# Optimization experiments

Measured on AMD Instinct MI355X. Metric: run time of the kernel, lower is better.

Reference implementation:

```python
import jax, jax.numpy as jnp
import numpy as np

D = 16  # attention temperature
COEF = 1.0 / float(np.sqrt(D))


def squash2(x, axis=-1):
    sq = jnp.sum(x * x, axis=axis, keepdims=True)
    norm = jnp.sqrt(sq)
    # (1 - 1/exp(||x||)) * x / sqrt(||x||^2 + 1e-8)
    return (1.0 - jnp.exp(-norm)) * x / jnp.sqrt(sq + 1e-8)


def setup_inputs() -> dict:
    key = jax.random.key(0)
    k1, k2, k3 = jax.random.split(key, 3)
    batch, in_caps, in_dim, num_caps, dim_caps = 128, 1024, 16, 16, 16
    x = jax.random.normal(k1, (batch, in_caps, in_dim), dtype=jnp.float32)
    W = 0.01 * jax.random.normal(k2, (1, num_caps, in_caps, dim_caps, in_dim), dtype=jnp.float32)
    B = 0.01 * jax.random.normal(k3, (num_caps, 1, in_caps), dtype=jnp.float32)
    return {"x": x, "W": W, "B": B}


def reference(x, W, B):
    # u_hat[b,n,c,d] = W[n,c,d,:] . x[b,c,:]
    u_hat = jnp.einsum('ncdi,bci->bncd', W[0], x)
    # a = coef * u_hat @ u_hat^T is only consumed via a.sum(dim=-2);
    # sum_r <u_hat[r], u_hat[k]> == <sum_r u_hat[r], u_hat[k]> (same math, no [c,c] matrix)
    scores = COEF * jnp.einsum('bnd,bnkd->bnk', u_hat.sum(axis=2), u_hat)  # [b,n,c]
    c = jax.nn.softmax(scores[:, :, None, :], axis=1)  # softmax over num_caps, [b,n,1,c]
    # s = (c + B) @ u_hat, squeeze row dim
    s = jnp.einsum('bnrc,bncd->bnrd', c + B[None], u_hat)[:, :, 0, :]  # [b,n,d]
    return squash2(s)
```

## Files before the change

kernel.cpp:

```cpp
#include <hip/hip_runtime.h>
#include <math.h>

#define NB 128
#define NC 1024
#define NN 16
#define ND 16
#define NI 16
#define COEF 0.25f

typedef __attribute__((ext_vector_type(8))) short short8;
typedef __attribute__((ext_vector_type(4))) float f32x4;
typedef unsigned short ushort_t;

__device__ __forceinline__ unsigned short f2bf(float f) {
  unsigned int u = __builtin_bit_cast(unsigned int, f);
  u += 0x7fffu + ((u >> 16) & 1u);
  return (unsigned short)(u >> 16);
}

__global__ __launch_bounds__(256) void k_prep(const float4* __restrict__ x,
                                              const float4* __restrict__ W,
                                              ushort_t* __restrict__ xb,
                                              ushort_t* __restrict__ Wb) {
  int id = blockIdx.x * 256 + threadIdx.x;
  const float4* src;
  ushort_t* dst;
  int k;
  if (id < 262144) { src = x; dst = xb; k = id; }
  else { src = W; dst = Wb; k = id - 262144; }
  float4 a = src[2 * k], b = src[2 * k + 1];
  short8 o;
  o[0] = (short)f2bf(a.x); o[1] = (short)f2bf(a.y);
  o[2] = (short)f2bf(a.z); o[3] = (short)f2bf(a.w);
  o[4] = (short)f2bf(b.x); o[5] = (short)f2bf(b.y);
  o[6] = (short)f2bf(b.z); o[7] = (short)f2bf(b.w);
  *(short8*)(dst + (size_t)k * 8) = o;
}

__global__ __launch_bounds__(1024) void k_usum(const ushort_t* __restrict__ xb,
                                               const ushort_t* __restrict__ Wb,
                                               float* __restrict__ usum2) {
  __shared__ f32x4 red[16][64];
  int bx = blockIdx.x;
  int n = bx >> 4, bt = (bx >> 1) & 7, h = bx & 1;
  int w = threadIdx.x >> 6, l = threadIdx.x & 63;
  int q = l >> 4, b16 = l & 15;
  int c0 = h * 512 + w * 32;
  const ushort_t* ap0 = Wb + (((size_t)(n * NC + c0 + (q >> 1)) * ND + b16) * NI) + (q & 1) * 8;
  const ushort_t* bp0 = xb + (size_t)(bt * 16 + b16) * (NC * NI) + (c0 + (q >> 1)) * NI + (q & 1) * 8;
  const ushort_t* ap1 = ap0 + 16 * ND * NI;
  const ushort_t* bp1 = bp0 + 16 * NI;
  f32x4 acc0 = {0.f, 0.f, 0.f, 0.f};
  f32x4 acc1 = {0.f, 0.f, 0.f, 0.f};
#pragma unroll
  for (int s = 0; s < 8; ++s) {
    short8 a0 = *(const short8*)ap0;
    short8 b0 = *(const short8*)bp0;
    short8 a1 = *(const short8*)ap1;
    short8 b1 = *(const short8*)bp1;
    acc0 = __builtin_amdgcn_mfma_f32_16x16x32_bf16(a0, b0, acc0, 0, 0, 0);
    acc1 = __builtin_amdgcn_mfma_f32_16x16x32_bf16(a1, b1, acc1, 0, 0, 0);
    ap0 += 2 * ND * NI; bp0 += 2 * NI;
    ap1 += 2 * ND * NI; bp1 += 2 * NI;
  }
  red[w][l] = acc0 + acc1;
  __syncthreads();
  if (threadIdx.x < 64) {
    f32x4 t = red[0][l];
#pragma unroll
    for (int k = 1; k < 16; ++k) t += red[k][l];
    *(f32x4*)(usum2 + (((size_t)h * NN + n) * NB + bt * 16 + b16) * ND + q * 4) = t;
  }
}

__global__ __launch_bounds__(512, 4) void k_bc(const ushort_t* __restrict__ xb,
                                               const ushort_t* __restrict__ Wb,
                                               const float* __restrict__ usum2,
                                               const float* __restrict__ Bbias,
                                               float* __restrict__ part) {
  __shared__ ushort_t Wl[NN][8][ND][NI];
  __shared__ ushort_t xl[16][136];
  __shared__ float scl[NN][8][16];
  int bx = blockIdx.x;
  int bt = bx >> 7, cc = bx & 127;
  int t = threadIdx.x;
  int w = t >> 6, l = t & 63;
  int q = l >> 4, b16 = l & 15;
  int c0 = cc * 8;
  int n0 = w, n1 = w + 8;

  {
    ushort_t* Wflat = &Wl[0][0][0][0];
    const ushort_t* Wsrc = Wb + (size_t)c0 * (ND * NI);
#pragma unroll
    for (int r = 0; r < 8; ++r) {
      int g = r * 512 + t;
      int n = g >> 8, rem = g & 255;
      *(short8*)(Wflat + n * 2048 + rem * 8) =
          *(const short8*)(Wsrc + (size_t)n * (NC * ND * NI) + rem * 8);
    }
    if (t < 256) {
      int b = t >> 4, j = t & 15;
      int c = j >> 1, i8 = j & 1;
      *(short8*)(&xl[b][c * 16 + i8 * 8]) =
          *(const short8*)(xb + ((size_t)(bt * 16 + b) * NC + c0 + c) * NI + i8 * 8);
    }
  }

  const float* u0p = usum2 + ((size_t)n0 * NB + bt * 16 + b16) * ND + q * 4;
  f32x4 us0 = *(const f32x4*)u0p + *(const f32x4*)(u0p + (size_t)NN * NB * ND);
  const float* u1p = usum2 + ((size_t)n1 * NB + bt * 16 + b16) * ND + q * 4;
  f32x4 us1 = *(const f32x4*)u1p + *(const f32x4*)(u1p + (size_t)NN * NB * ND);

  __syncthreads();

  f32x4 t0[8], t1[8];

#pragma unroll
  for (int c = 0; c < 8; ++c) {
    short8 av = {0, 0, 0, 0, 0, 0, 0, 0};
    short8 bv = {0, 0, 0, 0, 0, 0, 0, 0};
    if (q < 2) {
      av = *(const short8*)(&Wl[n0][c][b16][q * 8]);
      bv = *(const short8*)(&xl[b16][c * 16 + q * 8]);
    }
    f32x4 z = {0.f, 0.f, 0.f, 0.f};
    f32x4 d = __builtin_amdgcn_mfma_f32_16x16x32_bf16(av, bv, z, 0, 0, 0);
    t0[c] = d;
    float v = us0[0] * d[0] + us0[1] * d[1] + us0[2] * d[2] + us0[3] * d[3];
    v += __shfl_xor(v, 16);
    v += __shfl_xor(v, 32);
    if (l < 16) scl[n0][c][l] = COEF * v;
  }
#pragma unroll
  for (int c = 0; c < 8; ++c) {
    short8 av = {0, 0, 0, 0, 0, 0, 0, 0};
    short8 bv = {0, 0, 0, 0, 0, 0, 0, 0};
    if (q < 2) {
      av = *(const short8*)(&Wl[n1][c][b16][q * 8]);
      bv = *(const short8*)(&xl[b16][c * 16 + q * 8]);
    }
    f32x4 z = {0.f, 0.f, 0.f, 0.f};
    f32x4 d = __builtin_amdgcn_mfma_f32_16x16x32_bf16(av, bv, z, 0, 0, 0);
    t1[c] = d;
    float v = us1[0] * d[0] + us1[1] * d[1] + us1[2] * d[2] + us1[3] * d[3];
    v += __shfl_xor(v, 16);
    v += __shfl_xor(v, 32);
    if (l < 16) scl[n1][c][l] = COEF * v;
  }
  __syncthreads();

  if (t < 128) {
    int c = t >> 4, b = t & 15;
    float v[NN];
    float m = -1e30f;
#pragma unroll
    for (int k = 0; k < NN; ++k) {
      v[k] = scl[k][c][b];
      m = fmaxf(m, v[k]);
    }
    float sum = 0.f;
#pragma unroll
    for (int k = 0; k < NN; ++k) {
      v[k] = expf(v[k] - m);
      sum += v[k];
    }
    float inv = 1.0f / sum;
#pragma unroll
    for (int k = 0; k < NN; ++k) {
      scl[k][c][b] = v[k] * inv + Bbias[k * NC + c0 + c];
    }
  }
  __syncthreads();

  f32x4 acc0 = {0.f, 0.f, 0.f, 0.f};
  f32x4 acc1 = {0.f, 0.f, 0.f, 0.f};
#pragma unroll
  for (int c = 0; c < 8; ++c) {
    float cf0 = scl[n0][c][b16];
    float cf1 = scl[n1][c][b16];
    acc0[0] = fmaf(cf0, t0[c][0], acc0[0]);
    acc0[1] = fmaf(cf0, t0[c][1], acc0[1]);
    acc0[2] = fmaf(cf0, t0[c][2], acc0[2]);
    acc0[3] = fmaf(cf0, t0[c][3], acc0[3]);
    acc1[0] = fmaf(cf1, t1[c][0], acc1[0]);
    acc1[1] = fmaf(cf1, t1[c][1], acc1[1]);
    acc1[2] = fmaf(cf1, t1[c][2], acc1[2]);
    acc1[3] = fmaf(cf1, t1[c][3], acc1[3]);
  }
  *(f32x4*)(part + ((size_t)((n0 * 8 + bt) * 128 + cc)) * 256 + b16 * 16 + q * 4) = acc0;
  *(f32x4*)(part + ((size_t)((n1 * 8 + bt) * 128 + cc)) * 256 + b16 * 16 + q * 4) = acc1;
}

__global__ __launch_bounds__(256) void k_fin(const float* __restrict__ part,
                                             float* __restrict__ out) {
  int id2 = blockIdx.x * 256 + threadIdx.x;
  int h = id2 & 1;
  int id = id2 >> 1;
  int dq = id & 3, n = (id >> 2) & 15, b = id >> 6;
  int bt = b >> 4, b16 = b & 15;
  f32x4 sv = {0.f, 0.f, 0.f, 0.f};
  const float* pp = part + ((size_t)((n * 8 + bt) * 128 + h * 64)) * 256 + b16 * 16 + dq * 4;
  for (int k = 0; k < 64; ++k) {
    sv += *(const f32x4*)pp;
    pp += 256;
  }
  sv[0] += __shfl_xor(sv[0], 1);
  sv[1] += __shfl_xor(sv[1], 1);
  sv[2] += __shfl_xor(sv[2], 1);
  sv[3] += __shfl_xor(sv[3], 1);
  float sq = sv[0] * sv[0] + sv[1] * sv[1] + sv[2] * sv[2] + sv[3] * sv[3];
  sq += __shfl_xor(sq, 2);
  sq += __shfl_xor(sq, 4);
  float norm = sqrtf(sq);
  float scale = (1.0f - expf(-norm)) / sqrtf(sq + 1e-8f);
  if (h == 0) {
    f32x4 o = {sv[0] * scale, sv[1] * scale, sv[2] * scale, sv[3] * scale};
    *(f32x4*)(out + (size_t)id * 4) = o;
  }
}

extern "C" void kernel_launch(void* const* d_in, const int* in_sizes, int n_in,
                              void* d_out, int out_size, void* d_ws, size_t ws_size,
                              hipStream_t stream) {
  const float* x = (const float*)d_in[0];
  const float* W = (const float*)d_in[1];
  const float* Bb = (const float*)d_in[2];
  float* out = (float*)d_out;
  float* ws = (float*)d_ws;

  ushort_t* xb = (ushort_t*)ws;
  ushort_t* Wb = (ushort_t*)(ws + 1048576);
  float* part = ws + 1048576 + 2097152;
  float* usum2 = part + 4194304;

  hipLaunchKernelGGL(k_prep, dim3(3072), dim3(256), 0, stream,
                     (const float4*)x, (const float4*)W, xb, Wb);
  hipLaunchKernelGGL(k_usum, dim3(256), dim3(1024), 0, stream, xb, Wb, usum2);
  hipLaunchKernelGGL(k_bc, dim3(1024), dim3(512), 0, stream, xb, Wb, usum2, Bb, part);
  hipLaunchKernelGGL(k_fin, dim3(64), dim3(256), 0, stream, part, out);
}
```

Measured before the change: 48.31 us.

## Reuse staged W tile across four batch tiles and add MFMA accumulators

k_bc now loads its W slice into shared memory once per block and loops over four batch tiles, shrinking the grid from 1024 to 256 blocks. This is meant to cut the redundant global-to-LDS loads of W. k_usum remaps blocks batch-major and splits accumulation into four independent MFMA chains for more instruction-level parallelism. The cost is less parallelism and serialized per-tile phases inside each k_bc block.

Result: slower. 60.44 us (+25.1%).

```diff
diff --git a/kernel.cpp b/kernel.cpp
--- a/kernel.cpp
+++ b/kernel.cpp
@@ -42,28 +42,30 @@
                                                float* __restrict__ usum2) {
   __shared__ f32x4 red[16][64];
   int bx = blockIdx.x;
-  int n = bx >> 4, bt = (bx >> 1) & 7, h = bx & 1;
+  int bt = bx >> 5, g = bx & 31;
+  int n = g >> 1, h = g & 1;
   int w = threadIdx.x >> 6, l = threadIdx.x & 63;
   int q = l >> 4, b16 = l & 15;
   int c0 = h * 512 + w * 32;
-  const ushort_t* ap0 = Wb + (((size_t)(n * NC + c0 + (q >> 1)) * ND + b16) * NI) + (q & 1) * 8;
-  const ushort_t* bp0 = xb + (size_t)(bt * 16 + b16) * (NC * NI) + (c0 + (q >> 1)) * NI + (q & 1) * 8;
-  const ushort_t* ap1 = ap0 + 16 * ND * NI;
-  const ushort_t* bp1 = bp0 + 16 * NI;
-  f32x4 acc0 = {0.f, 0.f, 0.f, 0.f};
-  f32x4 acc1 = {0.f, 0.f, 0.f, 0.f};
-#pragma unroll
-  for (int s = 0; s < 8; ++s) {
-    short8 a0 = *(const short8*)ap0;
-    short8 b0 = *(const short8*)bp0;
-    short8 a1 = *(const short8*)ap1;
-    short8 b1 = *(const short8*)bp1;
-    acc0 = __builtin_amdgcn_mfma_f32_16x16x32_bf16(a0, b0, acc0, 0, 0, 0);
-    acc1 = __builtin_amdgcn_mfma_f32_16x16x32_bf16(a1, b1, acc1, 0, 0, 0);
-    ap0 += 2 * ND * NI; bp0 += 2 * NI;
-    ap1 += 2 * ND * NI; bp1 += 2 * NI;
-  }
-  red[w][l] = acc0 + acc1;
+  f32x4 acc[4];
+#pragma unroll
+  for (int kk = 0; kk < 4; ++kk) acc[kk] = (f32x4){0.f, 0.f, 0.f, 0.f};
+#pragma unroll
+  for (int kk = 0; kk < 4; ++kk) {
+    const ushort_t* ap =
+        Wb + (((size_t)(n * NC + c0 + kk * 8 + (q >> 1)) * ND + b16) * NI) + (q & 1) * 8;
+    const ushort_t* bp =
+        xb + (size_t)(bt * 16 + b16) * (NC * NI) + (c0 + kk * 8 + (q >> 1)) * NI + (q & 1) * 8;
+#pragma unroll
+    for (int s = 0; s < 4; ++s) {
+      short8 av = *(const short8*)ap;
+      short8 bv = *(const short8*)bp;
+      acc[kk] = __builtin_amdgcn_mfma_f32_16x16x32_bf16(av, bv, acc[kk], 0, 0, 0);
+      ap += 2 * ND * NI;
+      bp += 2 * NI;
+    }
+  }
+  red[w][l] = (acc[0] + acc[1]) + (acc[2] + acc[3]);
   __syncthreads();
   if (threadIdx.x < 64) {
     f32x4 t = red[0][l];
@@ -82,7 +84,7 @@
   __shared__ ushort_t xl[16][136];
   __shared__ float scl[NN][8][16];
   int bx = blockIdx.x;
-  int bt = bx >> 7, cc = bx & 127;
+  int btg = bx >> 7, cc = bx & 127;
   int t = threadIdx.x;
   int w = t >> 6, l = t & 63;
   int q = l >> 4, b16 = l & 15;
@@ -94,102 +96,104 @@
     const ushort_t* Wsrc = Wb + (size_t)c0 * (ND * NI);
 #pragma unroll
     for (int r = 0; r < 8; ++r) {
-      int g = r * 512 + t;
-      int n = g >> 8, rem = g & 255;
+      int gg = r * 512 + t;
+      int n = gg >> 8, rem = gg & 255;
       *(short8*)(Wflat + n * 2048 + rem * 8) =
           *(const short8*)(Wsrc + (size_t)n * (NC * ND * NI) + rem * 8);
     }
+  }
+
+  for (int j = 0; j < 4; ++j) {
+    int bt = btg * 4 + j;
     if (t < 256) {
-      int b = t >> 4, j = t & 15;
-      int c = j >> 1, i8 = j & 1;
+      int b = t >> 4, jj = t & 15;
+      int c = jj >> 1, i8 = jj & 1;
       *(short8*)(&xl[b][c * 16 + i8 * 8]) =
           *(const short8*)(xb + ((size_t)(bt * 16 + b) * NC + c0 + c) * NI + i8 * 8);
     }
-  }
-
-  const float* u0p = usum2 + ((size_t)n0 * NB + bt * 16 + b16) * ND + q * 4;
-  f32x4 us0 = *(const f32x4*)u0p + *(const f32x4*)(u0p + (size_t)NN * NB * ND);
-  const float* u1p = usum2 + ((size_t)n1 * NB + bt * 16 + b16) * ND + q * 4;
-  f32x4 us1 = *(const f32x4*)u1p + *(const f32x4*)(u1p + (size_t)NN * NB * ND);
-
-  __syncthreads();
-
-  f32x4 t0[8], t1[8];
-
-#pragma unroll
-  for (int c = 0; c < 8; ++c) {
-    short8 av = {0, 0, 0, 0, 0, 0, 0, 0};
-    short8 bv = {0, 0, 0, 0, 0, 0, 0, 0};
-    if (q < 2) {
-      av = *(const short8*)(&Wl[n0][c][b16][q * 8]);
-      bv = *(const short8*)(&xl[b16][c * 16 + q * 8]);
-    }
-    f32x4 z = {0.f, 0.f, 0.f, 0.f};
-    f32x4 d = __builtin_amdgcn_mfma_f32_16x16x32_bf16(av, bv, z, 0, 0, 0);
-    t0[c] = d;
-    float v = us0[0] * d[0] + us0[1] * d[1] + us0[2] * d[2] + us0[3] * d[3];
-    v += __shfl_xor(v, 16);
-    v += __shfl_xor(v, 32);
-    if (l < 16) scl[n0][c][l] = COEF * v;
-  }
-#pragma unroll
-  for (int c = 0; c < 8; ++c) {
-    short8 av = {0, 0, 0, 0, 0, 0, 0, 0};
-    short8 bv = {0, 0, 0, 0, 0, 0, 0, 0};
-    if (q < 2) {
-      av = *(const short8*)(&Wl[n1][c][b16][q * 8]);
-      bv = *(const short8*)(&xl[b16][c * 16 + q * 8]);
-    }
-    f32x4 z = {0.f, 0.f, 0.f, 0.f};
-    f32x4 d = __builtin_amdgcn_mfma_f32_16x16x32_bf16(av, bv, z, 0, 0, 0);
-    t1[c] = d;
-    float v = us1[0] * d[0] + us1[1] * d[1] + us1[2] * d[2] + us1[3] * d[3];
-    v += __shfl_xor(v, 16);
-    v += __shfl_xor(v, 32);
-    if (l < 16) scl[n1][c][l] = COEF * v;
-  }
-  __syncthreads();
-
-  if (t < 128) {
-    int c = t >> 4, b = t & 15;
-    float v[NN];
-    float m = -1e30f;
-#pragma unroll
-    for (int k = 0; k < NN; ++k) {
-      v[k] = scl[k][c][b];
-      m = fmaxf(m, v[k]);
-    }
-    float sum = 0.f;
-#pragma unroll
-    for (int k = 0; k < NN; ++k) {
-      v[k] = expf(v[k] - m);
-      sum += v[k];
-    }
-    float inv = 1.0f / sum;
-#pragma unroll
-    for (int k = 0; k < NN; ++k) {
-      scl[k][c][b] = v[k] * inv + Bbias[k * NC + c0 + c];
-    }
-  }
-  __syncthreads();
-
-  f32x4 acc0 = {0.f, 0.f, 0.f, 0.f};
-  f32x4 acc1 = {0.f, 0.f, 0.f, 0.f};
-#pragma unroll
-  for (int c = 0; c < 8; ++c) {
-    float cf0 = scl[n0][c][b16];
-    float cf1 = scl[n1][c][b16];
-    acc0[0] = fmaf(cf0, t0[c][0], acc0[0]);
-    acc0[1] = fmaf(cf0, t0[c][1], acc0[1]);
-    acc0[2] = fmaf(cf0, t0[c][2], acc0[2]);
-    acc0[3] = fmaf(cf0, t0[c][3], acc0[3]);
-    acc1[0] = fmaf(cf1, t1[c][0], acc1[0]);
-    acc1[1] = fmaf(cf1, t1[c][1], acc1[1]);
-    acc1[2] = fmaf(cf1, t1[c][2], acc1[2]);
-    acc1[3] = fmaf(cf1, t1[c][3], acc1[3]);
-  }
-  *(f32x4*)(part + ((size_t)((n0 * 8 + bt) * 128 + cc)) * 256 + b16 * 16 + q * 4) = acc0;
-  *(f32x4*)(part + ((size_t)((n1 * 8 + bt) * 128 + cc)) * 256 + b16 * 16 + q * 4) = acc1;
+    const float* u0p = usum2 + ((size_t)n0 * NB + bt * 16 + b16) * ND + q * 4;
+    f32x4 us0 = *(const f32x4*)u0p + *(const f32x4*)(u0p + (size_t)NN * NB * ND);
+    const float* u1p = usum2 + ((size_t)n1 * NB + bt * 16 + b16) * ND + q * 4;
+    f32x4 us1 = *(const f32x4*)u1p + *(const f32x4*)(u1p + (size_t)NN * NB * ND);
+    __syncthreads();
+
+    f32x4 t0[8], t1[8];
+
+#pragma unroll
+    for (int c = 0; c < 8; ++c) {
+      short8 av = {0, 0, 0, 0, 0, 0, 0, 0};
+      short8 bv = {0, 0, 0, 0, 0, 0, 0, 0};
+      if (q < 2) {
+        av = *(const short8*)(&Wl[n0][c][b16][q * 8]);
+        bv = *(const short8*)(&xl[b16][c * 16 + q * 8]);
+      }
+      f32x4 z = {0.f, 0.f, 0.f, 0.f};
+      f32x4 d = __builtin_amdgcn_mfma_f32_16x16x32_bf16(av, bv, z, 0, 0, 0);
+      t0[c] = d;
+      float v = us0[0] * d[0] + us0[1] * d[1] + us0[2] * d[2] + us0[3] * d[3];
+      v += __shfl_xor(v, 16);
+      v += __shfl_xor(v, 32);
+      if (l < 16) scl[n0][c][l] = COEF * v;
+    }
+#pragma unroll
+    for (int c = 0; c < 8; ++c) {
+      short8 av = {0, 0, 0, 0, 0, 0, 0, 0};
+      short8 bv = {0, 0, 0, 0, 0, 0, 0, 0};
+      if (q < 2) {
+        av = *(const short8*)(&Wl[n1][c][b16][q * 8]);
+        bv = *(const short8*)(&xl[b16][c * 16 + q * 8]);
+      }
+      f32x4 z = {0.f, 0.f, 0.f, 0.f};
+      f32x4 d = __builtin_amdgcn_mfma_f32_16x16x32_bf16(av, bv, z, 0, 0, 0);
+      t1[c] = d;
+      float v = us1[0] * d[0] + us1[1] * d[1] + us1[2] * d[2] + us1[3] * d[3];
+      v += __shfl_xor(v, 16);
+      v += __shfl_xor(v, 32);
+      if (l < 16) scl[n1][c][l] = COEF * v;
+    }
+    __syncthreads();
+
+    if (t < 128) {
+      int c = t >> 4, b = t & 15;
+      float v[NN];
+      float m = -1e30f;
+#pragma unroll
+      for (int k = 0; k < NN; ++k) {
+        v[k] = scl[k][c][b];
+        m = fmaxf(m, v[k]);
+      }
+      float sum = 0.f;
+#pragma unroll
+      for (int k = 0; k < NN; ++k) {
+        v[k] = expf(v[k] - m);
+        sum += v[k];
+      }
+      float inv = 1.0f / sum;
+#pragma unroll
+      for (int k = 0; k < NN; ++k) {
+        scl[k][c][b] = v[k] * inv + Bbias[k * NC + c0 + c];
+      }
+    }
+    __syncthreads();
+
+    f32x4 acc0 = {0.f, 0.f, 0.f, 0.f};
+    f32x4 acc1 = {0.f, 0.f, 0.f, 0.f};
+#pragma unroll
+    for (int c = 0; c < 8; ++c) {
+      float cf0 = scl[n0][c][b16];
+      float cf1 = scl[n1][c][b16];
+      acc0[0] = fmaf(cf0, t0[c][0], acc0[0]);
+      acc0[1] = fmaf(cf0, t0[c][1], acc0[1]);
+      acc0[2] = fmaf(cf0, t0[c][2], acc0[2]);
+      acc0[3] = fmaf(cf0, t0[c][3], acc0[3]);
+      acc1[0] = fmaf(cf1, t1[c][0], acc1[0]);
+      acc1[1] = fmaf(cf1, t1[c][1], acc1[1]);
+      acc1[2] = fmaf(cf1, t1[c][2], acc1[2]);
+      acc1[3] = fmaf(cf1, t1[c][3], acc1[3]);
+    }
+    *(f32x4*)(part + ((size_t)((n0 * 8 + bt) * 128 + cc)) * 256 + b16 * 16 + q * 4) = acc0;
+    *(f32x4*)(part + ((size_t)((n1 * 8 + bt) * 128 + cc)) * 256 + b16 * 16 + q * 4) = acc1;
+  }
 }
 
 __global__ __launch_bounds__(256) void k_fin(const float* __restrict__ part,
@@ -237,6 +241,6 @@
   hipLaunchKernelGGL(k_prep, dim3(3072), dim3(256), 0, stream,
                      (const float4*)x, (const float4*)W, xb, Wb);
   hipLaunchKernelGGL(k_usum, dim3(256), dim3(1024), 0, stream, xb, Wb, usum2);
-  hipLaunchKernelGGL(k_bc, dim3(1024), dim3(512), 0, stream, xb, Wb, usum2, Bb, part);
+  hipLaunchKernelGGL(k_bc, dim3(256), dim3(512), 0, stream, xb, Wb, usum2, Bb, part);
   hipLaunchKernelGGL(k_fin, dim3(64), dim3(256), 0, stream, part, out);
 }
```
